# Kernel tuning notes

Measured on AMD Instinct MI355X. Metric: run time of the kernel, lower is better.

## Reference

```python
import jax, jax.numpy as jnp
import numpy as np

B, C, HW, SCALE = 8, 512, 64, 8
M = C // SCALE  # Q/K channel dim
EPS = 1e-6


def setup_inputs() -> dict:
    key = jax.random.key(0)
    ks = jax.random.split(key, 8)
    s = 0.02
    return {
        "x": jax.random.normal(ks[0], (B, C, HW, HW), dtype=jnp.float32),
        "wq": jax.random.normal(ks[1], (M, C), dtype=jnp.float32) * s,
        "bq": jax.random.normal(ks[2], (M,), dtype=jnp.float32) * s,
        "wk": jax.random.normal(ks[3], (M, C), dtype=jnp.float32) * s,
        "bk": jax.random.normal(ks[4], (M,), dtype=jnp.float32) * s,
        "wv": jax.random.normal(ks[5], (C, C), dtype=jnp.float32) * s,
        "bv": jax.random.normal(ks[6], (C,), dtype=jnp.float32) * s,
        "gamma": jax.random.normal(ks[7], (1,), dtype=jnp.float32),
    }


def reference(x, wq, bq, wk, bk, wv, bv, gamma):
    b, c, w, h = x.shape
    n = w * h
    xf = x.reshape(b, c, n)  # [B,C,N]
    # 1x1 convs == channel GEMMs
    Q = jnp.einsum('bcn,mc->bmn', xf, wq) + bq[None, :, None]  # [B,M,N]
    K = jnp.einsum('bcn,mc->bmn', xf, wk) + bk[None, :, None]  # [B,M,N]
    V = jnp.einsum('bcn,oc->bon', xf, wv) + bv[None, :, None]  # [B,C,N]
    # pooling gate: global max + global avg over spatial dims -> [B,C,1]
    gate = (jnp.max(xf, axis=-1) + jnp.mean(xf, axis=-1))[:, :, None]
    V = gate * V
    Qf = jax.nn.softplus(Q).transpose(0, 2, 1)  # [B,N,M]
    Kf = jax.nn.softplus(K)                      # [B,M,N]
    KV = jnp.einsum('bmn,bcn->bmc', Kf, V)       # [B,M,C]
    norm = 1.0 / jnp.einsum('bnm,bm->bn', Qf, jnp.sum(Kf, axis=-1) + EPS)  # [B,N]
    wval = jnp.einsum('bnm,bmc,bn->bcn', Qf, KV, norm)  # [B,C,N]
    wval = wval.reshape(b, c, h, w)
    return x + gamma * wval
```

## Files before the change

### kernel.cpp

```cpp
#include <hip/hip_runtime.h>
#include <math.h>

#define Bb 8
#define Cc 512
#define Nn 4096
#define Mm 64
#define OC 640
#define EPSf 1e-6f

typedef unsigned short ushort_t;
typedef unsigned int uint_t;
typedef __attribute__((ext_vector_type(8))) short short8;
typedef __attribute__((ext_vector_type(4))) float f32x4;

constexpr size_t OFF_GATE = 0;
constexpr size_t OFF_BCAT = OFF_GATE + (size_t)Bb * Cc;
constexpr size_t OFF_GPM  = OFF_BCAT + (size_t)OC;
constexpr size_t OFF_GPS  = OFF_GPM + (size_t)64 * Bb * Cc;
constexpr size_t OFF_WBF  = OFF_GPS + (size_t)64 * Bb * Cc;
constexpr size_t OFF_XT   = OFF_WBF + (size_t)OC * Cc / 2;
constexpr size_t OFF_QBF  = OFF_XT + (size_t)Bb * Nn * Cc / 2;
constexpr size_t OFF_KBF  = OFF_QBF + (size_t)Bb * Mm * Nn / 2;
constexpr size_t OFF_VBF  = OFF_KBF + (size_t)Bb * Mm * Nn / 2;
constexpr size_t OFF_KVT  = OFF_VBF + (size_t)Bb * Cc * Nn / 2;
constexpr size_t OFF_KSUM = OFF_KVT + (size_t)Bb * Cc * Mm;
constexpr size_t OFF_NORM = OFF_KSUM + (size_t)Bb * Mm;

__device__ __forceinline__ float softplus_f(float v) {
    return fmaxf(v, 0.f) + __logf(1.f + __expf(-fabsf(v)));
}
__device__ __forceinline__ ushort_t f2bf(float f) {
    uint_t u = __float_as_uint(f);
    uint_t r = (u + 0x7fffu + ((u >> 16) & 1u)) >> 16;
    return (ushort_t)r;
}
__device__ __forceinline__ float bf2f(ushort_t h) {
    return __uint_as_float(((uint_t)h) << 16);
}
__device__ __forceinline__ void gload_lds16(const void* g, void* l) {
    __builtin_amdgcn_global_load_lds(
        (const __attribute__((address_space(1))) unsigned int*)g,
        (__attribute__((address_space(3))) unsigned int*)l, 16, 0, 0);
}
#define BARRIER()   asm volatile("s_barrier" ::: "memory")
#define WAIT_VM(N)  asm volatile("s_waitcnt vmcnt(" #N ")" ::: "memory")

__global__ void wconv_k(const float* __restrict__ wq, const float* __restrict__ bq,
                        const float* __restrict__ wk, const float* __restrict__ bk,
                        const float* __restrict__ wv, const float* __restrict__ bv,
                        ushort_t* __restrict__ wbf, float* __restrict__ bcat) {
    int i = blockIdx.x * 256 + threadIdx.x;
    if (i < OC * Cc) {
        int o = i / Cc, c = i % Cc;
        float v;
        if (o < Mm)            v = wq[o * Cc + c];
        else if (o < 2 * Mm)   v = wk[(o - Mm) * Cc + c];
        else                   v = wv[(o - 2 * Mm) * Cc + c];
        wbf[i] = f2bf(v);
    }
    if (i < OC) {
        float v;
        if (i < Mm)            v = bq[i];
        else if (i < 2 * Mm)   v = bk[i - Mm];
        else                   v = bv[i - 2 * Mm];
        bcat[i] = v;
    }
}

__global__ __launch_bounds__(256) void xtrans_k(const float* __restrict__ x, ushort_t* __restrict__ xT,
                                                float* __restrict__ gpm, float* __restrict__ gps) {
    const int nb = blockIdx.x * 64;
    const int cb = blockIdx.y * 64;
    const int b  = blockIdx.z;
    __shared__ float Xt[64][65];
    __shared__ float pmx[4][64], psm[4][64];
    const int t = threadIdx.x;
    #pragma unroll
    for (int r = 0; r < 16; r++) {
        int cl = (t >> 6) + r * 4;
        int nl = t & 63;
        Xt[cl][nl] = x[((size_t)b * Cc + cb + cl) * Nn + nb + nl];
    }
    __syncthreads();
    #pragma unroll
    for (int r = 0; r < 8; r++) {
        int nl = (t >> 5) + r * 8;
        int c0 = (t & 31) * 2;
        uint_t pk = (uint_t)f2bf(Xt[c0][nl]) | ((uint_t)f2bf(Xt[c0 + 1][nl]) << 16);
        *(uint_t*)(xT + ((size_t)b * Nn + nb + nl) * Cc + cb + c0) = pk;
    }
    {
        int cl = t & 63, q = t >> 6;
        float mx = -3.4e38f, sm = 0.f;
        #pragma unroll
        for (int j = 0; j < 16; j++) {
            float v = Xt[cl][q * 16 + j];
            mx = fmaxf(mx, v); sm += v;
        }
        pmx[q][cl] = mx; psm[q][cl] = sm;
    }
    __syncthreads();
    if (t < 64) {
        float mx = fmaxf(fmaxf(pmx[0][t], pmx[1][t]), fmaxf(pmx[2][t], pmx[3][t]));
        float sm = psm[0][t] + psm[1][t] + psm[2][t] + psm[3][t];
        size_t idx = (size_t)blockIdx.x * (Bb * Cc) + (size_t)b * Cc + cb + t;
        gpm[idx] = mx;
        gps[idx] = sm;
    }
}

__global__ void gatered_k(const float* __restrict__ gpm, const float* __restrict__ gps,
                          float* __restrict__ gate) {
    int bc = blockIdx.x;
    int l = threadIdx.x;
    float mx = gpm[(size_t)l * (Bb * Cc) + bc];
    float sm = gps[(size_t)l * (Bb * Cc) + bc];
    #pragma unroll
    for (int off = 32; off; off >>= 1) {
        mx = fmaxf(mx, __shfl_xor(mx, off));
        sm += __shfl_xor(sm, off);
    }
    if (l == 0) gate[bc] = mx + sm * (1.f / Nn);
}

__global__ __launch_bounds__(256, 3) void qkv_mfma_k(const ushort_t* __restrict__ wbf,
                                                     const ushort_t* __restrict__ xT,
                                                     const float* __restrict__ bcat,
                                                     const float* __restrict__ gate,
                                                     ushort_t* __restrict__ Qbf,
                                                     ushort_t* __restrict__ Kbf,
                                                     ushort_t* __restrict__ Vbf) {
    const int nb = blockIdx.x * 128;
    const int ob = blockIdx.y * 128;
    const int b  = blockIdx.z;
    __shared__ ushort_t At[2][4096];
    __shared__ ushort_t Bt[2][4096];
    const int tid  = threadIdx.x;
    const int w    = tid >> 6;
    const int lane = tid & 63;
    const int wr   = w >> 1, wc = w & 1;
    const int hi   = lane >> 4, lo = lane & 15;
    const int rwl  = lane >> 2;
    const int kc   = (((lane & 3) ^ ((lane >> 3) & 3)) * 8);
    const int sx   = (hi ^ ((lo >> 1) & 3)) * 8;
    const ushort_t* xb = xT + (size_t)b * Nn * Cc;

    f32x4 acc[4][4] = {};

    auto stage = [&](int buf, int kb) {
        #pragma unroll
        for (int li = 0; li < 2; li++) {
            const int rw = (w * 2 + li) * 16 + rwl;
            gload_lds16(wbf + (size_t)(ob + rw) * Cc + kb + kc, &At[buf][(w * 2 + li) * 512]);
            gload_lds16(xb + (size_t)(nb + rw) * Cc + kb + kc, &Bt[buf][(w * 2 + li) * 512]);
        }
    };
    auto compute = [&](int buf) {
        short8 a[4], bfr[4];
        #pragma unroll
        for (int mi = 0; mi < 4; mi++)
            a[mi] = *(const short8*)(&At[buf][(wr * 64 + mi * 16 + lo) * 32 + sx]);
        #pragma unroll
        for (int ni = 0; ni < 4; ni++)
            bfr[ni] = *(const short8*)(&Bt[buf][(wc * 64 + ni * 16 + lo) * 32 + sx]);
        #pragma unroll
        for (int mi = 0; mi < 4; mi++)
            #pragma unroll
            for (int ni = 0; ni < 4; ni++)
                acc[mi][ni] = __builtin_amdgcn_mfma_f32_16x16x32_bf16(a[mi], bfr[ni], acc[mi][ni], 0, 0, 0);
    };

    stage(0, 0);
    #pragma unroll
    for (int t = 0; t < 16; ++t) {
        if (t < 15) {
            stage((t + 1) & 1, (t + 1) * 32);
            WAIT_VM(4);
        } else {
            WAIT_VM(0);
        }
        BARRIER();
        compute(t & 1);
        BARRIER();
    }

    #pragma unroll
    for (int mi = 0; mi < 4; mi++) {
        #pragma unroll
        for (int r = 0; r < 4; r++) {
            const int o = ob + wr * 64 + mi * 16 + hi * 4 + r;
            const float bias = bcat[o];
            if (o < Mm) {
                ushort_t* dst = Qbf + ((size_t)b * Mm + o) * Nn;
                #pragma unroll
                for (int ni = 0; ni < 4; ni++)
                    dst[nb + wc * 64 + ni * 16 + lo] = f2bf(softplus_f(acc[mi][ni][r] + bias));
            } else if (o < 2 * Mm) {
                ushort_t* dst = Kbf + ((size_t)b * Mm + (o - Mm)) * Nn;
                #pragma unroll
                for (int ni = 0; ni < 4; ni++)
                    dst[nb + wc * 64 + ni * 16 + lo] = f2bf(softplus_f(acc[mi][ni][r] + bias));
            } else {
                const int c = o - 2 * Mm;
                const float g = gate[b * Cc + c];
                ushort_t* dst = Vbf + ((size_t)b * Cc + c) * Nn;
                #pragma unroll
                for (int ni = 0; ni < 4; ni++)
                    dst[nb + wc * 64 + ni * 16 + lo] = f2bf(g * (acc[mi][ni][r] + bias));
            }
        }
    }
}

__global__ __launch_bounds__(256) void ksum_k(const ushort_t* __restrict__ Kbf, float* __restrict__ Ksum) {
    int bm = blockIdx.x;
    const ushort_t* row = Kbf + (size_t)bm * Nn;
    int t = threadIdx.x;
    float sm = 0.f;
    for (int i = t * 8; i < Nn; i += 2048) {
        short8 v = *(const short8*)(row + i);
        #pragma unroll
        for (int j = 0; j < 8; j++) sm += bf2f((ushort_t)v[j]);
    }
    #pragma unroll
    for (int off = 32; off; off >>= 1) sm += __shfl_xor(sm, off);
    __shared__ float ssm[4];
    if ((t & 63) == 0) ssm[t >> 6] = sm;
    __syncthreads();
    if (t == 0) Ksum[bm] = ssm[0] + ssm[1] + ssm[2] + ssm[3];
}

__global__ __launch_bounds__(256, 3) void kv_mfma_k(const ushort_t* __restrict__ Kbf,
                                                    const ushort_t* __restrict__ Vbf,
                                                    float* __restrict__ KVpart) {
    const int cb = blockIdx.x * 128;
    const int split = blockIdx.y;
    const int b = blockIdx.z;
    __shared__ ushort_t Vt[2][4096];
    __shared__ ushort_t Kt[2][2048];
    const int tid = threadIdx.x;
    const int w = tid >> 6, lane = tid & 63;
    const int hi = lane >> 4, lo = lane & 15;
    const int rwl = lane >> 2;
    const int kc  = (((lane & 3) ^ ((lane >> 3) & 3)) * 8);
    const int sx  = (hi ^ ((lo >> 1) & 3)) * 8;
    const ushort_t* Vb = Vbf + (size_t)b * Cc * Nn;
    const ushort_t* Kb = Kbf + (size_t)b * Mm * Nn;
    const int nbase = split * 512;

    f32x4 acc[2][4] = {};

    auto stage = [&](int buf, int n0) {
        #pragma unroll
        for (int li = 0; li < 2; li++) {
            const int rw = (w * 2 + li) * 16 + rwl;
            gload_lds16(Vb + (size_t)(cb + rw) * Nn + n0 + kc, &Vt[buf][(w * 2 + li) * 512]);
        }
        gload_lds16(Kb + (size_t)(w * 16 + rwl) * Nn + n0 + kc, &Kt[buf][w * 512]);
    };
    auto compute = [&](int buf) {
        short8 a[2], bv[4];
        #pragma unroll
        for (int mi = 0; mi < 2; mi++)
            a[mi] = *(const short8*)(&Vt[buf][(w * 32 + mi * 16 + lo) * 32 + sx]);
        #pragma unroll
        for (int ni = 0; ni < 4; ni++)
            bv[ni] = *(const short8*)(&Kt[buf][(ni * 16 + lo) * 32 + sx]);
        #pragma unroll
        for (int mi = 0; mi < 2; mi++)
            #pragma unroll
            for (int ni = 0; ni < 4; ni++)
                acc[mi][ni] = __builtin_amdgcn_mfma_f32_16x16x32_bf16(a[mi], bv[ni], acc[mi][ni], 0, 0, 0);
    };

    stage(0, nbase);
    #pragma unroll
    for (int t = 0; t < 16; ++t) {
        if (t < 15) {
            stage((t + 1) & 1, nbase + (t + 1) * 32);
            WAIT_VM(3);
        } else {
            WAIT_VM(0);
        }
        BARRIER();
        compute(t & 1);
        BARRIER();
    }

    float* dst = KVpart + (size_t)(split * Bb + b) * Cc * Mm;
    #pragma unroll
    for (int mi = 0; mi < 2; mi++)
        #pragma unroll
        for (int r = 0; r < 4; r++) {
            const int c = cb + w * 32 + mi * 16 + hi * 4 + r;
            #pragma unroll
            for (int ni = 0; ni < 4; ni++)
                dst[(size_t)c * Mm + ni * 16 + lo] = acc[mi][ni][r];
        }
}

__global__ __launch_bounds__(256) void kvred_k(const float* __restrict__ KVpart, float* __restrict__ KVT) {
    int i = blockIdx.x * 256 + threadIdx.x;
    const f32x4* p = (const f32x4*)KVpart;
    f32x4 s = p[i];
    #pragma unroll
    for (int sp = 1; sp < 8; sp++) s += p[(size_t)sp * 65536 + i];
    ((f32x4*)KVT)[i] = s;
}

__global__ __launch_bounds__(256) void norm_k(const ushort_t* __restrict__ Qbf,
                                              const float* __restrict__ Ksum,
                                              float* __restrict__ normb) {
    int b = blockIdx.y;
    int n = blockIdx.x * 256 + threadIdx.x;
    __shared__ float ks[Mm];
    if (threadIdx.x < Mm) ks[threadIdx.x] = Ksum[b * Mm + threadIdx.x] + EPSf;
    __syncthreads();
    float s = 0.f;
    #pragma unroll 8
    for (int m = 0; m < Mm; m++) s += bf2f(Qbf[((size_t)b * Mm + m) * Nn + n]) * ks[m];
    normb[(size_t)b * Nn + n] = 1.f / s;
}

__global__ __launch_bounds__(256) void final_k(const float* __restrict__ x,
                                               const ushort_t* __restrict__ Qbf,
                                               const float* __restrict__ KVT,
                                               const float* __restrict__ normb,
                                               const float* __restrict__ gamma,
                                               float* __restrict__ out) {
    const int nb = blockIdx.x * 64;
    const int cb = blockIdx.y * 64;
    const int b  = blockIdx.z;
    __shared__ float Qt[64][65];
    __shared__ float KVt[64][65];
    const int tid = threadIdx.x;
    const int tr = tid >> 4, tc = tid & 15;

    #pragma unroll
    for (int r = 0; r < 16; r++) {
        int a = (tid >> 6) + r * 4;
        int bl = tid & 63;
        Qt[a][bl]  = bf2f(Qbf[((size_t)b * Mm + a) * Nn + nb + bl]);
        KVt[bl][a] = KVT[((size_t)b * Cc + cb + a) * Mm + bl];
    }
    __syncthreads();
    float acc[4][4] = {};
    #pragma unroll 8
    for (int k = 0; k < 64; k++) {
        float a0 = KVt[k][tr * 4 + 0], a1 = KVt[k][tr * 4 + 1];
        float a2 = KVt[k][tr * 4 + 2], a3 = KVt[k][tr * 4 + 3];
        float b0 = Qt[k][tc * 4 + 0], b1 = Qt[k][tc * 4 + 1];
        float b2 = Qt[k][tc * 4 + 2], b3 = Qt[k][tc * 4 + 3];
        acc[0][0] += a0 * b0; acc[0][1] += a0 * b1; acc[0][2] += a0 * b2; acc[0][3] += a0 * b3;
        acc[1][0] += a1 * b0; acc[1][1] += a1 * b1; acc[1][2] += a1 * b2; acc[1][3] += a1 * b3;
        acc[2][0] += a2 * b0; acc[2][1] += a2 * b1; acc[2][2] += a2 * b2; acc[2][3] += a2 * b3;
        acc[3][0] += a3 * b0; acc[3][1] += a3 * b1; acc[3][2] += a3 * b2; acc[3][3] += a3 * b3;
    }
    const float g = gamma[0];
    const int n0 = nb + tc * 4;
    float4 nrm = *(const float4*)(normb + (size_t)b * Nn + n0);
    #pragma unroll
    for (int i = 0; i < 4; i++) {
        int c = cb + tr * 4 + i;
        size_t idx = ((size_t)b * Cc + c) * Nn + n0;
        float4 xv = *(const float4*)(x + idx);
        float4 o;
        o.x = xv.x + g * nrm.x * acc[i][0];
        o.y = xv.y + g * nrm.y * acc[i][1];
        o.z = xv.z + g * nrm.z * acc[i][2];
        o.w = xv.w + g * nrm.w * acc[i][3];
        *(float4*)(out + idx) = o;
    }
}

extern "C" void kernel_launch(void* const* d_in, const int* in_sizes, int n_in,
                              void* d_out, int out_size, void* d_ws, size_t ws_size,
                              hipStream_t stream) {
    const float* x     = (const float*)d_in[0];
    const float* wq    = (const float*)d_in[1];
    const float* bq    = (const float*)d_in[2];
    const float* wk    = (const float*)d_in[3];
    const float* bk    = (const float*)d_in[4];
    const float* wv    = (const float*)d_in[5];
    const float* bv    = (const float*)d_in[6];
    const float* gamma = (const float*)d_in[7];
    float* out = (float*)d_out;
    float* ws  = (float*)d_ws;

    float*    gate   = ws + OFF_GATE;
    float*    bcat   = ws + OFF_BCAT;
    float*    gpm    = ws + OFF_GPM;
    float*    gps    = ws + OFF_GPS;
    ushort_t* wbf    = (ushort_t*)(ws + OFF_WBF);
    ushort_t* xT     = (ushort_t*)(ws + OFF_XT);
    float*    KVpart = ws + OFF_XT;
    ushort_t* Qbf    = (ushort_t*)(ws + OFF_QBF);
    ushort_t* Kbf    = (ushort_t*)(ws + OFF_KBF);
    ushort_t* Vbf    = (ushort_t*)(ws + OFF_VBF);
    float*    KVT    = ws + OFF_KVT;
    float*    Ksum   = ws + OFF_KSUM;
    float*    normb  = ws + OFF_NORM;

    wconv_k<<<(OC * Cc + 255) / 256, 256, 0, stream>>>(wq, bq, wk, bk, wv, bv, wbf, bcat);
    xtrans_k<<<dim3(Nn / 64, Cc / 64, Bb), 256, 0, stream>>>(x, xT, gpm, gps);
    gatered_k<<<Bb * Cc, 64, 0, stream>>>(gpm, gps, gate);
    qkv_mfma_k<<<dim3(Nn / 128, OC / 128, Bb), 256, 0, stream>>>(wbf, xT, bcat, gate, Qbf, Kbf, Vbf);
    ksum_k<<<Bb * Mm, 256, 0, stream>>>(Kbf, Ksum);
    kv_mfma_k<<<dim3(Cc / 128, 8, Bb), 256, 0, stream>>>(Kbf, Vbf, KVpart);
    kvred_k<<<(Bb * Cc * Mm / 4) / 256, 256, 0, stream>>>(KVpart, KVT);
    norm_k<<<dim3(Nn / 256, Bb), 256, 0, stream>>>(Qbf, Ksum, normb);
    final_k<<<dim3(Nn / 64, Cc / 64, Bb), 256, 0, stream>>>(x, Qbf, KVT, normb, gamma, out);
}
```

Baseline: 133.4 us.

## Move final Q·KV product to bf16 MFMA with transposed Q and fused norm

Replaces the fp32 scalar FMA final kernel with a bf16 MFMA kernel on 128x128 tiles. KV is now stored in bf16, and a new kernel transposes Q to [N,M] bf16 while also computing the normaliser. LDS is filled via swizzled global_load_lds. This removes FP32 ALU work from the final stage, at the cost of an extra transpose pass and reduced precision for KV.

```diff
diff --git a/kernel.cpp b/kernel.cpp
--- a/kernel.cpp
+++ b/kernel.cpp
@@ -22,9 +22,10 @@
 constexpr size_t OFF_QBF  = OFF_XT + (size_t)Bb * Nn * Cc / 2;
 constexpr size_t OFF_KBF  = OFF_QBF + (size_t)Bb * Mm * Nn / 2;
 constexpr size_t OFF_VBF  = OFF_KBF + (size_t)Bb * Mm * Nn / 2;
-constexpr size_t OFF_KVT  = OFF_VBF + (size_t)Bb * Cc * Nn / 2;
-constexpr size_t OFF_KSUM = OFF_KVT + (size_t)Bb * Cc * Mm;
+constexpr size_t OFF_KVBF = OFF_VBF + (size_t)Bb * Cc * Nn / 2;
+constexpr size_t OFF_KSUM = OFF_KVBF + (size_t)Bb * Cc * Mm / 2;
 constexpr size_t OFF_NORM = OFF_KSUM + (size_t)Bb * Mm;
+constexpr size_t OFF_QT   = OFF_NORM + (size_t)Bb * Nn;
 
 __device__ __forceinline__ float softplus_f(float v) {
     return fmaxf(v, 0.f) + __logf(1.f + __expf(-fabsf(v)));
@@ -299,77 +300,128 @@
         }
 }
 
-__global__ __launch_bounds__(256) void kvred_k(const float* __restrict__ KVpart, float* __restrict__ KVT) {
+__global__ __launch_bounds__(256) void kvred_k(const float* __restrict__ KVpart, ushort_t* __restrict__ KVbf) {
     int i = blockIdx.x * 256 + threadIdx.x;
     const f32x4* p = (const f32x4*)KVpart;
     f32x4 s = p[i];
     #pragma unroll
     for (int sp = 1; sp < 8; sp++) s += p[(size_t)sp * 65536 + i];
-    ((f32x4*)KVT)[i] = s;
-}
-
-__global__ __launch_bounds__(256) void norm_k(const ushort_t* __restrict__ Qbf,
-                                              const float* __restrict__ Ksum,
-                                              float* __restrict__ normb) {
-    int b = blockIdx.y;
-    int n = blockIdx.x * 256 + threadIdx.x;
-    __shared__ float ks[Mm];
-    if (threadIdx.x < Mm) ks[threadIdx.x] = Ksum[b * Mm + threadIdx.x] + EPSf;
-    __syncthreads();
-    float s = 0.f;
-    #pragma unroll 8
-    for (int m = 0; m < Mm; m++) s += bf2f(Qbf[((size_t)b * Mm + m) * Nn + n]) * ks[m];
-    normb[(size_t)b * Nn + n] = 1.f / s;
-}
-
-__global__ __launch_bounds__(256) void final_k(const float* __restrict__ x,
-                                               const ushort_t* __restrict__ Qbf,
-                                               const float* __restrict__ KVT,
-                                               const float* __restrict__ normb,
-                                               const float* __restrict__ gamma,
-                                               float* __restrict__ out) {
-    const int nb = blockIdx.x * 64;
-    const int cb = blockIdx.y * 64;
+    uint2 pk;
+    pk.x = (uint_t)f2bf(s[0]) | ((uint_t)f2bf(s[1]) << 16);
+    pk.y = (uint_t)f2bf(s[2]) | ((uint_t)f2bf(s[3]) << 16);
+    *(uint2*)(KVbf + (size_t)i * 4) = pk;
+}
+
+__global__ __launch_bounds__(256) void qtransnorm_k(const ushort_t* __restrict__ Qbf,
+                                                    const float* __restrict__ Ksum,
+                                                    ushort_t* __restrict__ QT,
+                                                    float* __restrict__ normb) {
+    const int n0 = blockIdx.x * 64;
+    const int b  = blockIdx.y;
+    __shared__ float Qs[64][65];
+    __shared__ float ks[64];
+    __shared__ float ps[4][64];
+    const int t = threadIdx.x;
+    if (t < 64) ks[t] = Ksum[b * Mm + t] + EPSf;
+    {
+        int m = t >> 2, q = t & 3;
+        const ushort_t* src = Qbf + ((size_t)b * Mm + m) * Nn + n0 + q * 16;
+        short8 v0 = *(const short8*)(src);
+        short8 v1 = *(const short8*)(src + 8);
+        #pragma unroll
+        for (int j = 0; j < 8; j++) {
+            Qs[m][q * 16 + j]     = bf2f((ushort_t)v0[j]);
+            Qs[m][q * 16 + 8 + j] = bf2f((ushort_t)v1[j]);
+        }
+    }
+    __syncthreads();
+    {
+        int n = t & 63, ch = t >> 6;
+        float s = 0.f;
+        #pragma unroll
+        for (int j = 0; j < 16; j++) s += Qs[ch * 16 + j][n] * ks[ch * 16 + j];
+        ps[ch][n] = s;
+    }
+    __syncthreads();
+    if (t < 64) normb[(size_t)b * Nn + n0 + t] = 1.f / (ps[0][t] + ps[1][t] + ps[2][t] + ps[3][t]);
+    #pragma unroll
+    for (int i = 0; i < 2; i++) {
+        int u = t + i * 256;
+        int n = u >> 3, j = u & 7;
+        short8 v;
+        #pragma unroll
+        for (int jj = 0; jj < 8; jj++) v[jj] = (short)f2bf(Qs[j * 8 + jj][n]);
+        *(short8*)(QT + ((size_t)b * Nn + n0 + n) * Mm + j * 8) = v;
+    }
+}
+
+__global__ __launch_bounds__(256, 2) void final_mfma_k(const float* __restrict__ x,
+                                                       const ushort_t* __restrict__ QT,
+                                                       const ushort_t* __restrict__ KVbf,
+                                                       const float* __restrict__ normb,
+                                                       const float* __restrict__ gamma,
+                                                       float* __restrict__ out) {
+    const int nb = blockIdx.x * 128;
+    const int cb = blockIdx.y * 128;
     const int b  = blockIdx.z;
-    __shared__ float Qt[64][65];
-    __shared__ float KVt[64][65];
-    const int tid = threadIdx.x;
-    const int tr = tid >> 4, tc = tid & 15;
-
-    #pragma unroll
-    for (int r = 0; r < 16; r++) {
-        int a = (tid >> 6) + r * 4;
-        int bl = tid & 63;
-        Qt[a][bl]  = bf2f(Qbf[((size_t)b * Mm + a) * Nn + nb + bl]);
-        KVt[bl][a] = KVT[((size_t)b * Cc + cb + a) * Mm + bl];
-    }
-    __syncthreads();
-    float acc[4][4] = {};
-    #pragma unroll 8
-    for (int k = 0; k < 64; k++) {
-        float a0 = KVt[k][tr * 4 + 0], a1 = KVt[k][tr * 4 + 1];
-        float a2 = KVt[k][tr * 4 + 2], a3 = KVt[k][tr * 4 + 3];
-        float b0 = Qt[k][tc * 4 + 0], b1 = Qt[k][tc * 4 + 1];
-        float b2 = Qt[k][tc * 4 + 2], b3 = Qt[k][tc * 4 + 3];
-        acc[0][0] += a0 * b0; acc[0][1] += a0 * b1; acc[0][2] += a0 * b2; acc[0][3] += a0 * b3;
-        acc[1][0] += a1 * b0; acc[1][1] += a1 * b1; acc[1][2] += a1 * b2; acc[1][3] += a1 * b3;
-        acc[2][0] += a2 * b0; acc[2][1] += a2 * b1; acc[2][2] += a2 * b2; acc[2][3] += a2 * b3;
-        acc[3][0] += a3 * b0; acc[3][1] += a3 * b1; acc[3][2] += a3 * b2; acc[3][3] += a3 * b3;
-    }
+    __shared__ ushort_t Qs[128 * 64];
+    __shared__ ushort_t Ks[128 * 64];
+    const int tid  = threadIdx.x;
+    const int w    = tid >> 6;
+    const int lane = tid & 63;
+    const int wr   = w >> 1, wc = w & 1;
+    const int hi   = lane >> 4, lo = lane & 15;
+    const int lr   = lane >> 3;
+    const int swz  = (((lane & 7) ^ (lr & 7)) * 8);
+    const ushort_t* Qb = QT + (size_t)b * Nn * Mm;
+    const ushort_t* Kb = KVbf + (size_t)b * Cc * Mm;
+
+    #pragma unroll
+    for (int p = 0; p < 4; p++) {
+        const int rb = p * 32 + w * 8;
+        gload_lds16(Qb + (size_t)(nb + rb + lr) * Mm + swz, &Qs[rb * 64]);
+        gload_lds16(Kb + (size_t)(cb + rb + lr) * Mm + swz, &Ks[rb * 64]);
+    }
+    __syncthreads();
+
+    f32x4 acc[4][4] = {};
+    #pragma unroll
+    for (int kk = 0; kk < 2; kk++) {
+        short8 a[4], bfr[4];
+        #pragma unroll
+        for (int mi = 0; mi < 4; mi++) {
+            const int row = wr * 64 + mi * 16 + lo;
+            a[mi] = *(const short8*)(&Qs[row * 64 + (((kk * 4 + hi) ^ (lo & 7)) * 8)]);
+        }
+        #pragma unroll
+        for (int ni = 0; ni < 4; ni++) {
+            const int row = wc * 64 + ni * 16 + lo;
+            bfr[ni] = *(const short8*)(&Ks[row * 64 + (((kk * 4 + hi) ^ (lo & 7)) * 8)]);
+        }
+        #pragma unroll
+        for (int mi = 0; mi < 4; mi++)
+            #pragma unroll
+            for (int ni = 0; ni < 4; ni++)
+                acc[mi][ni] = __builtin_amdgcn_mfma_f32_16x16x32_bf16(a[mi], bfr[ni], acc[mi][ni], 0, 0, 0);
+    }
+
     const float g = gamma[0];
-    const int n0 = nb + tc * 4;
-    float4 nrm = *(const float4*)(normb + (size_t)b * Nn + n0);
-    #pragma unroll
-    for (int i = 0; i < 4; i++) {
-        int c = cb + tr * 4 + i;
-        size_t idx = ((size_t)b * Cc + c) * Nn + n0;
-        float4 xv = *(const float4*)(x + idx);
-        float4 o;
-        o.x = xv.x + g * nrm.x * acc[i][0];
-        o.y = xv.y + g * nrm.y * acc[i][1];
-        o.z = xv.z + g * nrm.z * acc[i][2];
-        o.w = xv.w + g * nrm.w * acc[i][3];
-        *(float4*)(out + idx) = o;
+    #pragma unroll
+    for (int mi = 0; mi < 4; mi++) {
+        const int n0 = nb + wr * 64 + mi * 16 + hi * 4;
+        float4 nrm = *(const float4*)(normb + (size_t)b * Nn + n0);
+        #pragma unroll
+        for (int ni = 0; ni < 4; ni++) {
+            const int c = cb + wc * 64 + ni * 16 + lo;
+            size_t idx = ((size_t)b * Cc + c) * Nn + n0;
+            float4 xv = *(const float4*)(x + idx);
+            float4 o;
+            o.x = xv.x + g * nrm.x * acc[mi][ni][0];
+            o.y = xv.y + g * nrm.y * acc[mi][ni][1];
+            o.z = xv.z + g * nrm.z * acc[mi][ni][2];
+            o.w = xv.w + g * nrm.w * acc[mi][ni][3];
+            *(float4*)(out + idx) = o;
+        }
     }
 }
 
@@ -397,9 +449,10 @@
     ushort_t* Qbf    = (ushort_t*)(ws + OFF_QBF);
     ushort_t* Kbf    = (ushort_t*)(ws + OFF_KBF);
     ushort_t* Vbf    = (ushort_t*)(ws + OFF_VBF);
-    float*    KVT    = ws + OFF_KVT;
+    ushort_t* KVbf   = (ushort_t*)(ws + OFF_KVBF);
     float*    Ksum   = ws + OFF_KSUM;
     float*    normb  = ws + OFF_NORM;
+    ushort_t* QT     = (ushort_t*)(ws + OFF_QT);
 
     wconv_k<<<(OC * Cc + 255) / 256, 256, 0, stream>>>(wq, bq, wk, bk, wv, bv, wbf, bcat);
     xtrans_k<<<dim3(Nn / 64, Cc / 64, Bb), 256, 0, stream>>>(x, xT, gpm, gps);
@@ -407,7 +460,7 @@
     qkv_mfma_k<<<dim3(Nn / 128, OC / 128, Bb), 256, 0, stream>>>(wbf, xT, bcat, gate, Qbf, Kbf, Vbf);
     ksum_k<<<Bb * Mm, 256, 0, stream>>>(Kbf, Ksum);
     kv_mfma_k<<<dim3(Cc / 128, 8, Bb), 256, 0, stream>>>(Kbf, Vbf, KVpart);
-    kvred_k<<<(Bb * Cc * Mm / 4) / 256, 256, 0, stream>>>(KVpart, KVT);
-    norm_k<<<dim3(Nn / 256, Bb), 256, 0, stream>>>(Qbf, Ksum, normb);
-    final_k<<<dim3(Nn / 64, Cc / 64, Bb), 256, 0, stream>>>(x, Qbf, KVT, normb, gamma, out);
-}
+    kvred_k<<<(Bb * Cc * Mm / 4) / 256, 256, 0, stream>>>(KVpart, KVbf);
+    qtransnorm_k<<<dim3(Nn / 64, Bb), 256, 0, stream>>>(Qbf, Ksum, QT, normb);
+    final_mfma_k<<<dim3(Nn / 128, Cc / 128, Bb), 256, 0, stream>>>(x, QT, KVbf, normb, gamma, out);
+}
```

After: 114.2 us. 14.3% less time.
